# Optimization experiments

Measured on AMD Instinct MI355X. Metric: run time of the kernel, lower is better.

Reference implementation:

```python
import jax, jax.numpy as jnp
import numpy as np

N_NODES = 20000
N_EDGES = 320000
NUM_FEAT = 14
DIM = 256


def setup_inputs() -> dict:
    key = jax.random.key(0)
    ks = jax.random.split(key, 12)
    x = jax.random.normal(ks[0], (N_NODES, NUM_FEAT), dtype=jnp.float32)
    edge_index = jax.random.randint(ks[1], (2, N_EDGES), 0, N_NODES, dtype=jnp.int64)
    edge_weight = jax.random.uniform(ks[2], (N_EDGES,), dtype=jnp.float32)

    def lin_w(k, fan_in, fan_out):
        b = 1.0 / np.sqrt(fan_in)
        return jax.random.uniform(k, (fan_in, fan_out), jnp.float32, -b, b)

    params = {
        'W1_rel': lin_w(ks[3], NUM_FEAT, DIM), 'b1_rel': jnp.zeros((DIM,), jnp.float32),
        'W1_root': lin_w(ks[4], NUM_FEAT, DIM),
        'W2_rel': lin_w(ks[5], DIM, DIM), 'b2_rel': jnp.zeros((DIM,), jnp.float32),
        'W2_root': lin_w(ks[6], DIM, DIM),
        'W3_rel': lin_w(ks[7], DIM, DIM), 'b3_rel': jnp.zeros((DIM,), jnp.float32),
        'W3_root': lin_w(ks[8], DIM, DIM),
        'W_lin': lin_w(ks[9], 3 * DIM, DIM), 'b_lin': jnp.zeros((DIM,), jnp.float32),
    }
    return {'x': x, 'edge_index': edge_index, 'edge_weight': edge_weight, **params}


def _graph_conv(x, src, dst, ew, W_rel, b_rel, W_root, n_nodes):
    # message: x_j * w_ij ; aggr='mean' over incoming edges (count, not weight sum)
    msg = x[src] * ew[:, None]                               # [E, F]
    agg = jax.ops.segment_sum(msg, dst, num_segments=n_nodes)  # [N, F]
    cnt = jax.ops.segment_sum(jnp.ones_like(ew), dst, num_segments=n_nodes)
    mean = agg / jnp.maximum(cnt, 1.0)[:, None]
    return mean @ W_rel + b_rel + x @ W_root


def reference(x, edge_index, edge_weight,
              W1_rel, b1_rel, W1_root,
              W2_rel, b2_rel, W2_root,
              W3_rel, b3_rel, W3_root,
              W_lin, b_lin):
    src, dst = edge_index[0], edge_index[1]
    n = x.shape[0]
    # eval mode: dropout is identity
    x1 = jax.nn.relu(_graph_conv(x, src, dst, edge_weight, W1_rel, b1_rel, W1_root, n))
    x2 = jax.nn.relu(_graph_conv(x1, src, dst, edge_weight, W2_rel, b2_rel, W2_root, n))
    x3 = jax.nn.relu(_graph_conv(x2, src, dst, edge_weight, W3_rel, b3_rel, W3_root, n))
    xc = jnp.concatenate([x1, x2, x3], axis=-1)              # [N, 3*DIM]
    return xc @ W_lin + b_lin
```

## Files before the change

kernel.cpp:

```cpp
#include <hip/hip_runtime.h>

#define N_NODES 20000
#define N_EDGES 320000
#define NFEAT 14
#define DIM 256

typedef short bf16x8 __attribute__((ext_vector_type(8)));
typedef float f32x4 __attribute__((ext_vector_type(4)));

__device__ __forceinline__ float b2f(unsigned short u) {
    union { unsigned int u; float f; } v; v.u = ((unsigned int)u) << 16; return v.f;
}
__device__ __forceinline__ unsigned short f2b(float f) {
    union { float f; unsigned int u; } v; v.f = f;
    unsigned int r = v.u + 0x7fffu + ((v.u >> 16) & 1u);
    return (unsigned short)(r >> 16);
}


__global__ __launch_bounds__(256) void k_degree(const int* __restrict__ ei, int* __restrict__ cnt) {
    int e = blockIdx.x * 256 + threadIdx.x;
    if (e < N_EDGES) atomicAdd(&cnt[ei[N_EDGES + e]], 1);
}

__global__ __launch_bounds__(1024) void k_scan(const int* __restrict__ cnt,
                                               int* __restrict__ row_ptr,
                                               int* __restrict__ cursor) {
    __shared__ int wsums[16];
    __shared__ int carry;
    int tid = threadIdx.x;
    if (tid == 0) carry = 0;
    __syncthreads();
    for (int base = 0; base < N_NODES; base += 1024) {
        int i = base + tid;
        int v = (i < N_NODES) ? cnt[i] : 0;
        int lane = tid & 63, w = tid >> 6;
        int s = v;
        for (int o = 1; o < 64; o <<= 1) { int t = __shfl_up(s, o); if (lane >= o) s += t; }
        if (lane == 63) wsums[w] = s;
        __syncthreads();
        if (tid < 16) {
            int t = wsums[tid];
            for (int o = 1; o < 16; o <<= 1) { int u = __shfl_up(t, o); if (tid >= o) t += u; }
            wsums[tid] = t;
        }
        __syncthreads();
        int excl = carry + (w ? wsums[w - 1] : 0) + (s - v);
        if (i < N_NODES) { row_ptr[i] = excl; cursor[i] = excl; }
        __syncthreads();
        if (tid == 0) carry += wsums[15];
        __syncthreads();
    }
}

__global__ __launch_bounds__(256) void k_fill(const int* __restrict__ ei, const float* __restrict__ ew,
                                              int* __restrict__ cursor,
                                              int* __restrict__ csr_src, float* __restrict__ csr_w) {
    int e = blockIdx.x * 256 + threadIdx.x;
    if (e < N_EDGES) {
        int d = ei[N_EDGES + e];
        int p = atomicAdd(&cursor[d], 1);
        csr_src[p] = ei[e];
        csr_w[p] = ew[e];
    }
}


__global__ __launch_bounds__(256) void k_wstage(
    const float* __restrict__ W2r, const float* __restrict__ W2o,
    const float* __restrict__ W3r, const float* __restrict__ W3o,
    const float* __restrict__ Wl, unsigned short* __restrict__ out) {
    int part = blockIdx.x >> 8;
    int idx = (blockIdx.x & 255) * 256 + threadIdx.x;
    int s = idx >> 13, rem = idx & 8191, c = rem >> 5, j = rem & 31;
    const float* W; int koff = 0;
    switch (part) {
        case 0: W = W2r; break;
        case 1: W = W2o; break;
        case 2: W = W3r; break;
        case 3: W = W3o; break;
        default: W = Wl; koff = (part - 4) * 256; break;
    }
    out[(size_t)part * 65536 + idx] = f2b(W[(size_t)(koff + s * 32 + j) * 256 + c]);
}


__global__ __launch_bounds__(256) void k_layer1(
    const float* __restrict__ x, const int* __restrict__ row_ptr, const int* __restrict__ cnt,
    const int* __restrict__ csr_src, const float* __restrict__ csr_w,
    const float* __restrict__ Wrel, const float* __restrict__ brel, const float* __restrict__ Wroot,
    unsigned short* __restrict__ x1b) {
    __shared__ float sWrel[NFEAT][DIM];
    __shared__ float sWroot[NFEAT][DIM];
    __shared__ float sb[DIM];
    int tid = threadIdx.x;
    for (int i = tid; i < NFEAT * DIM; i += 256) {
        (&sWrel[0][0])[i] = Wrel[i];
        (&sWroot[0][0])[i] = Wroot[i];
    }
    if (tid < DIM) sb[tid] = brel[tid];
    __syncthreads();

    int wv = tid >> 6, lane = tid & 63;
    int node = blockIdx.x * 4 + wv;
    int start = row_ptr[node], deg = cnt[node];

    float acc[NFEAT];
#pragma unroll
    for (int k = 0; k < NFEAT; k++) acc[k] = 0.f;
    for (int e = start + lane; e < start + deg; e += 64) {
        int s = csr_src[e];
        float w = csr_w[e];
        const float2* xr2 = (const float2*)(x + (size_t)s * NFEAT);
#pragma unroll
        for (int k2 = 0; k2 < 7; k2++) {
            float2 v = xr2[k2];
            acc[2 * k2]     += v.x * w;
            acc[2 * k2 + 1] += v.y * w;
        }
    }
#pragma unroll
    for (int k = 0; k < NFEAT; k++) {
        float v = acc[k];
        v += __shfl_xor(v, 1);  v += __shfl_xor(v, 2);  v += __shfl_xor(v, 4);
        v += __shfl_xor(v, 8);  v += __shfl_xor(v, 16); v += __shfl_xor(v, 32);
        acc[k] = v;
    }
    float inv = 1.f / fmaxf((float)deg, 1.f);
    float xr[NFEAT];
#pragma unroll
    for (int k = 0; k < NFEAT; k++) { acc[k] *= inv; xr[k] = x[(size_t)node * NFEAT + k]; }

#pragma unroll
    for (int j = 0; j < 4; j++) {
        int d = lane + 64 * j;
        float o = sb[d];
#pragma unroll
        for (int k = 0; k < NFEAT; k++) o += acc[k] * sWrel[k][d] + xr[k] * sWroot[k][d];
        x1b[(size_t)node * DIM + d] = f2b(fmaxf(o, 0.f));
    }
}


__global__ __launch_bounds__(256) void k_spmm_mean(
    const unsigned short* __restrict__ xin, const int* __restrict__ row_ptr,
    const int* __restrict__ cnt, const int* __restrict__ csr_src,
    const float* __restrict__ csr_w, unsigned short* __restrict__ meanb) {
    int wv = threadIdx.x >> 6, lane = threadIdx.x & 63;
    int node = blockIdx.x * 4 + wv;
    int start = row_ptr[node], deg = cnt[node];
    float a0 = 0.f, a1 = 0.f, a2 = 0.f, a3 = 0.f;
    for (int e = start; e < start + deg; ++e) {
        int s = csr_src[e];
        float w = csr_w[e];
        ushort4 v = *(const ushort4*)(xin + (size_t)s * DIM + lane * 4);
        a0 += b2f(v.x) * w; a1 += b2f(v.y) * w; a2 += b2f(v.z) * w; a3 += b2f(v.w) * w;
    }
    float inv = 1.f / fmaxf((float)deg, 1.f);
    ushort4 o;
    o.x = f2b(a0 * inv); o.y = f2b(a1 * inv); o.z = f2b(a2 * inv); o.w = f2b(a3 * inv);
    *(ushort4*)(meanb + (size_t)node * DIM + lane * 4) = o;
}


__global__ __launch_bounds__(256) void k_gemm_mfma(
    const unsigned short* __restrict__ A0, const unsigned short* __restrict__ A1,
    const unsigned short* __restrict__ A2,
    const unsigned short* __restrict__ B0, const unsigned short* __restrict__ B1,
    const unsigned short* __restrict__ B2,
    int nparts, const float* __restrict__ bias,
    unsigned short* __restrict__ outb, float* __restrict__ outf, int do_relu) {
    __shared__ __align__(16) unsigned short Bs[256][40];
    int t = threadIdx.x;
    int l = t & 63, wv = t >> 6;
    int rowPanel = wv >> 1, colPanel = wv & 1;
    int row0 = blockIdx.x * 32;
    int lr = l & 15, kg = l >> 4;
    int row_a = row0 + rowPanel * 16 + lr;

    f32x4 acc[8];
#pragma unroll
    for (int i = 0; i < 8; i++) acc[i] = (f32x4){0.f, 0.f, 0.f, 0.f};

    for (int p = 0; p < nparts; ++p) {
        const unsigned short* A = (p == 0) ? A0 : (p == 1) ? A1 : A2;
        const unsigned short* B = (p == 0) ? B0 : (p == 1) ? B1 : B2;
        for (int s = 0; s < 8; ++s) {
            const int4* src = (const int4*)(B + (size_t)s * 8192 + (size_t)t * 32);
            int4 v0 = src[0], v1 = src[1], v2 = src[2], v3 = src[3];
            *(int4*)&Bs[t][0]  = v0;
            *(int4*)&Bs[t][8]  = v1;
            *(int4*)&Bs[t][16] = v2;
            *(int4*)&Bs[t][24] = v3;
            __syncthreads();
            bf16x8 a = *(const bf16x8*)(A + (size_t)row_a * DIM + s * 32 + kg * 8);
#pragma unroll
            for (int ct = 0; ct < 8; ++ct) {
                int col = colPanel * 128 + ct * 16 + lr;
                bf16x8 b = *(const bf16x8*)&Bs[col][kg * 8];
                acc[ct] = __builtin_amdgcn_mfma_f32_16x16x32_bf16(a, b, acc[ct], 0, 0, 0);
            }
            __syncthreads();
        }
    }

#pragma unroll
    for (int ct = 0; ct < 8; ++ct) {
        int col = colPanel * 128 + ct * 16 + lr;
        float bv = bias[col];
#pragma unroll
        for (int r = 0; r < 4; ++r) {
            int row = row0 + rowPanel * 16 + kg * 4 + r;
            float v = acc[ct][r] + bv;
            if (do_relu) v = fmaxf(v, 0.f);
            if (outb) outb[(size_t)row * DIM + col] = f2b(v);
            else      outf[(size_t)row * DIM + col] = v;
        }
    }
}


extern "C" void kernel_launch(void* const* d_in, const int* in_sizes, int n_in,
                              void* d_out, int out_size, void* d_ws, size_t ws_size,
                              hipStream_t stream) {
    (void)in_sizes; (void)n_in; (void)out_size; (void)ws_size;
    const float* x       = (const float*)d_in[0];
    const int*   ei      = (const int*)d_in[1];
    const float* ew      = (const float*)d_in[2];
    const float* W1_rel  = (const float*)d_in[3];
    const float* b1      = (const float*)d_in[4];
    const float* W1_root = (const float*)d_in[5];
    const float* W2_rel  = (const float*)d_in[6];
    const float* b2      = (const float*)d_in[7];
    const float* W2_root = (const float*)d_in[8];
    const float* W3_rel  = (const float*)d_in[9];
    const float* b3      = (const float*)d_in[10];
    const float* W3_root = (const float*)d_in[11];
    const float* W_lin   = (const float*)d_in[12];
    const float* b_lin   = (const float*)d_in[13];
    float* out = (float*)d_out;

    char* ws = (char*)d_ws;
    size_t off = 0;
    auto alloc = [&](size_t bytes) -> void* {
        off = (off + 255) & ~(size_t)255;
        void* p = ws + off;
        off += bytes;
        return p;
    };
    int*   cnt     = (int*)alloc((size_t)N_NODES * 4);
    int*   row_ptr = (int*)alloc((size_t)N_NODES * 4);
    int*   cursor  = (int*)alloc((size_t)N_NODES * 4);
    int*   csr_src = (int*)alloc((size_t)N_EDGES * 4);
    float* csr_w   = (float*)alloc((size_t)N_EDGES * 4);
    unsigned short* wst   = (unsigned short*)alloc((size_t)7 * 65536 * 2);
    unsigned short* meanb = (unsigned short*)alloc((size_t)N_NODES * DIM * 2);
    unsigned short* x1b   = (unsigned short*)alloc((size_t)N_NODES * DIM * 2);
    unsigned short* x2b   = (unsigned short*)alloc((size_t)N_NODES * DIM * 2);
    unsigned short* x3b   = (unsigned short*)alloc((size_t)N_NODES * DIM * 2);

    hipMemsetAsync(cnt, 0, (size_t)N_NODES * 4, stream);

    int eblocks = (N_EDGES + 255) / 256;
    k_degree<<<eblocks, 256, 0, stream>>>(ei, cnt);
    k_scan<<<1, 1024, 0, stream>>>(cnt, row_ptr, cursor);
    k_fill<<<eblocks, 256, 0, stream>>>(ei, ew, cursor, csr_src, csr_w);

    k_wstage<<<7 * 256, 256, 0, stream>>>(W2_rel, W2_root, W3_rel, W3_root, W_lin, wst);

    k_layer1<<<N_NODES / 4, 256, 0, stream>>>(x, row_ptr, cnt, csr_src, csr_w,
                                              W1_rel, b1, W1_root, x1b);

    const int ggrid = N_NODES / 32;

    k_spmm_mean<<<N_NODES / 4, 256, 0, stream>>>(x1b, row_ptr, cnt, csr_src, csr_w, meanb);
    k_gemm_mfma<<<ggrid, 256, 0, stream>>>(meanb, x1b, nullptr,
                                           wst, wst + 65536, nullptr,
                                           2, b2, x2b, nullptr, 1);

    k_spmm_mean<<<N_NODES / 4, 256, 0, stream>>>(x2b, row_ptr, cnt, csr_src, csr_w, meanb);
    k_gemm_mfma<<<ggrid, 256, 0, stream>>>(meanb, x2b, nullptr,
                                           wst + 2 * 65536, wst + 3 * 65536, nullptr,
                                           2, b3, x3b, nullptr, 1);

    k_gemm_mfma<<<ggrid, 256, 0, stream>>>(x1b, x2b, x3b,
                                           wst + 4 * 65536, wst + 5 * 65536, wst + 6 * 65536,
                                           3, b_lin, nullptr, out, 0);
}
```

Baseline: 345.8 us.

## Replace serial scan with atomic segment allocation, restructure layer1 and weight staging

The single-block prefix scan becomes a multi-block kernel in which each wavefront scans its 64 degrees and claims a contiguous range via an atomic on a global counter. CSR row segments are therefore no longer in node order, but each node still gets a correct private range. Weight staging now transposes through shared memory so reads and writes are coalesced, using 56 blocks instead of 1792. Layer 1 processes 32 nodes per block, with lanes split as 4 edges by 16 features, so weight loads into LDS are amortised and gathers are coalesced per row.

Measured after the change: 350.9 us. No clear change (+1.5%).

```diff
diff --git a/kernel.cpp b/kernel.cpp
--- a/kernel.cpp
+++ b/kernel.cpp
@@ -23,34 +23,21 @@
     if (e < N_EDGES) atomicAdd(&cnt[ei[N_EDGES + e]], 1);
 }
 
-__global__ __launch_bounds__(1024) void k_scan(const int* __restrict__ cnt,
+__global__ __launch_bounds__(256) void k_alloc(const int* __restrict__ cnt,
+                                               int* __restrict__ total,
                                                int* __restrict__ row_ptr,
                                                int* __restrict__ cursor) {
-    __shared__ int wsums[16];
-    __shared__ int carry;
-    int tid = threadIdx.x;
-    if (tid == 0) carry = 0;
-    __syncthreads();
-    for (int base = 0; base < N_NODES; base += 1024) {
-        int i = base + tid;
-        int v = (i < N_NODES) ? cnt[i] : 0;
-        int lane = tid & 63, w = tid >> 6;
-        int s = v;
-        for (int o = 1; o < 64; o <<= 1) { int t = __shfl_up(s, o); if (lane >= o) s += t; }
-        if (lane == 63) wsums[w] = s;
-        __syncthreads();
-        if (tid < 16) {
-            int t = wsums[tid];
-            for (int o = 1; o < 16; o <<= 1) { int u = __shfl_up(t, o); if (tid >= o) t += u; }
-            wsums[tid] = t;
-        }
-        __syncthreads();
-        int excl = carry + (w ? wsums[w - 1] : 0) + (s - v);
-        if (i < N_NODES) { row_ptr[i] = excl; cursor[i] = excl; }
-        __syncthreads();
-        if (tid == 0) carry += wsums[15];
-        __syncthreads();
-    }
+    int i = blockIdx.x * 256 + threadIdx.x;
+    int lane = threadIdx.x & 63;
+    int deg = (i < N_NODES) ? cnt[i] : 0;
+    int s = deg;
+    for (int o = 1; o < 64; o <<= 1) { int t = __shfl_up(s, o); if (lane >= o) s += t; }
+    int wsum = __shfl(s, 63);
+    int base = 0;
+    if (lane == 63) base = atomicAdd(total, wsum);
+    base = __shfl(base, 63);
+    int excl = base + s - deg;
+    if (i < N_NODES) { row_ptr[i] = excl; cursor[i] = excl; }
 }
 
 __global__ __launch_bounds__(256) void k_fill(const int* __restrict__ ei, const float* __restrict__ ew,
@@ -70,9 +57,9 @@
     const float* __restrict__ W2r, const float* __restrict__ W2o,
     const float* __restrict__ W3r, const float* __restrict__ W3o,
     const float* __restrict__ Wl, unsigned short* __restrict__ out) {
-    int part = blockIdx.x >> 8;
-    int idx = (blockIdx.x & 255) * 256 + threadIdx.x;
-    int s = idx >> 13, rem = idx & 8191, c = rem >> 5, j = rem & 31;
+    __shared__ unsigned short tb[256][33];
+    int part = blockIdx.x >> 3, s = blockIdx.x & 7;
+    int tid = threadIdx.x;
     const float* W; int koff = 0;
     switch (part) {
         case 0: W = W2r; break;
@@ -81,7 +68,17 @@
         case 3: W = W3o; break;
         default: W = Wl; koff = (part - 4) * 256; break;
     }
-    out[(size_t)part * 65536 + idx] = f2b(W[(size_t)(koff + s * 32 + j) * 256 + c]);
+#pragma unroll 4
+    for (int j = 0; j < 32; ++j) {
+        tb[tid][j] = f2b(W[(size_t)(koff + s * 32 + j) * 256 + tid]);
+    }
+    __syncthreads();
+    unsigned short* dst = out + (size_t)part * 65536 + (size_t)s * 8192;
+#pragma unroll 4
+    for (int i = 0; i < 32; ++i) {
+        int flat = i * 256 + tid;
+        dst[flat] = tb[flat >> 5][flat & 31];
+    }
 }
 
 
@@ -102,42 +99,41 @@
     __syncthreads();
 
     int wv = tid >> 6, lane = tid & 63;
-    int node = blockIdx.x * 4 + wv;
-    int start = row_ptr[node], deg = cnt[node];
-
-    float acc[NFEAT];
-#pragma unroll
-    for (int k = 0; k < NFEAT; k++) acc[k] = 0.f;
-    for (int e = start + lane; e < start + deg; e += 64) {
-        int s = csr_src[e];
-        float w = csr_w[e];
-        const float2* xr2 = (const float2*)(x + (size_t)s * NFEAT);
-#pragma unroll
-        for (int k2 = 0; k2 < 7; k2++) {
-            float2 v = xr2[k2];
-            acc[2 * k2]     += v.x * w;
-            acc[2 * k2 + 1] += v.y * w;
-        }
-    }
-#pragma unroll
-    for (int k = 0; k < NFEAT; k++) {
-        float v = acc[k];
-        v += __shfl_xor(v, 1);  v += __shfl_xor(v, 2);  v += __shfl_xor(v, 4);
-        v += __shfl_xor(v, 8);  v += __shfl_xor(v, 16); v += __shfl_xor(v, 32);
-        acc[k] = v;
-    }
-    float inv = 1.f / fmaxf((float)deg, 1.f);
-    float xr[NFEAT];
-#pragma unroll
-    for (int k = 0; k < NFEAT; k++) { acc[k] *= inv; xr[k] = x[(size_t)node * NFEAT + k]; }
-
-#pragma unroll
-    for (int j = 0; j < 4; j++) {
-        int d = lane + 64 * j;
-        float o = sb[d];
-#pragma unroll
-        for (int k = 0; k < NFEAT; k++) o += acc[k] * sWrel[k][d] + xr[k] * sWroot[k][d];
-        x1b[(size_t)node * DIM + d] = f2b(fmaxf(o, 0.f));
+    int esub = lane >> 4, k = lane & 15;
+    bool kval = (k < NFEAT);
+
+    for (int n8 = 0; n8 < 8; ++n8) {
+        int node = blockIdx.x * 32 + n8 * 4 + wv;
+        int start = row_ptr[node], deg = cnt[node];
+        int end = start + deg;
+
+        float acc = 0.f;
+        for (int e0 = start; e0 < end; e0 += 4) {
+            int e = e0 + esub;
+            if (e < end && kval) {
+                int s = csr_src[e];
+                acc += x[(size_t)s * NFEAT + k] * csr_w[e];
+            }
+        }
+        acc += __shfl_xor(acc, 16);
+        acc += __shfl_xor(acc, 32);
+        float macc = acc / fmaxf((float)deg, 1.f);
+
+        float av[NFEAT], xr[NFEAT];
+#pragma unroll
+        for (int k2 = 0; k2 < NFEAT; ++k2) av[k2] = __shfl(macc, k2);
+#pragma unroll
+        for (int k2 = 0; k2 < NFEAT; ++k2) xr[k2] = x[(size_t)node * NFEAT + k2];
+
+#pragma unroll
+        for (int j = 0; j < 4; ++j) {
+            int d = lane + 64 * j;
+            float o = sb[d];
+#pragma unroll
+            for (int k2 = 0; k2 < NFEAT; ++k2)
+                o += av[k2] * sWrel[k2][d] + xr[k2] * sWroot[k2][d];
+            x1b[(size_t)node * DIM + d] = f2b(fmaxf(o, 0.f));
+        }
     }
 }
 
@@ -248,7 +244,7 @@
         off += bytes;
         return p;
     };
-    int*   cnt     = (int*)alloc((size_t)N_NODES * 4);
+    int*   cnt     = (int*)alloc((size_t)(N_NODES + 1) * 4);
     int*   row_ptr = (int*)alloc((size_t)N_NODES * 4);
     int*   cursor  = (int*)alloc((size_t)N_NODES * 4);
     int*   csr_src = (int*)alloc((size_t)N_EDGES * 4);
@@ -258,18 +254,19 @@
     unsigned short* x1b   = (unsigned short*)alloc((size_t)N_NODES * DIM * 2);
     unsigned short* x2b   = (unsigned short*)alloc((size_t)N_NODES * DIM * 2);
     unsigned short* x3b   = (unsigned short*)alloc((size_t)N_NODES * DIM * 2);
-
-    hipMemsetAsync(cnt, 0, (size_t)N_NODES * 4, stream);
+    int* total = cnt + N_NODES;
+
+    hipMemsetAsync(cnt, 0, (size_t)(N_NODES + 1) * 4, stream);
 
     int eblocks = (N_EDGES + 255) / 256;
     k_degree<<<eblocks, 256, 0, stream>>>(ei, cnt);
-    k_scan<<<1, 1024, 0, stream>>>(cnt, row_ptr, cursor);
+    k_alloc<<<(N_NODES + 255) / 256, 256, 0, stream>>>(cnt, total, row_ptr, cursor);
     k_fill<<<eblocks, 256, 0, stream>>>(ei, ew, cursor, csr_src, csr_w);
 
-    k_wstage<<<7 * 256, 256, 0, stream>>>(W2_rel, W2_root, W3_rel, W3_root, W_lin, wst);
-
-    k_layer1<<<N_NODES / 4, 256, 0, stream>>>(x, row_ptr, cnt, csr_src, csr_w,
-                                              W1_rel, b1, W1_root, x1b);
+    k_wstage<<<56, 256, 0, stream>>>(W2_rel, W2_root, W3_rel, W3_root, W_lin, wst);
+
+    k_layer1<<<N_NODES / 32, 256, 0, stream>>>(x, row_ptr, cnt, csr_src, csr_w,
+                                               W1_rel, b1, W1_root, x1b);
 
     const int ggrid = N_NODES / 32;
 
```
